# Kernel tuning notes

Hardware: AMD Instinct MI355X
Metric: run time of the kernel (lower is better)

Reference implementation:

```python
import jax, jax.numpy as jnp
import numpy as np


def setup_inputs() -> dict:
    key = jax.random.key(0)
    k1, k2 = jax.random.split(key)
    B, H, W, C = 16, 1024, 1024, 3
    image = jax.random.normal(k1, (B, H, W, C), dtype=jnp.float32)
    flow = jax.random.normal(k2, (B, H, W, 2), dtype=jnp.float32)
    return {"image": image, "flow": flow}


def reference(image, flow):
    # Backward warp: out(p) = bilinear_sample(image, p + flow(p)).
    # NOTE: the original build() swaps width/height (width=shape[1], height=shape[2]);
    # this is only consistent for square images (H == W), which we assume here.
    B, H, W, C = image.shape
    grid_x = jnp.arange(W, dtype=jnp.float32)[None, None, :]  # [1,1,W]
    grid_y = jnp.arange(H, dtype=jnp.float32)[None, :, None]  # [1,H,1]
    x = grid_x + flow[..., 0]  # [B,H,W]
    y = grid_y + flow[..., 1]
    # normalize to [-1,1] then back (faithful to original round-trip)
    x = 0.5 * (2.0 * (x / W - 0.5) + 1.0) * W
    y = 0.5 * (2.0 * (y / H - 0.5) + 1.0) * H
    # corner indices (tf.cast truncates toward zero, as does astype(int32))
    x0 = x.astype(jnp.int32)
    x1 = x0 + 1
    y0 = y.astype(jnp.int32)
    y1 = y0 + 1
    x0 = jnp.clip(x0, 0, W - 1)
    x1 = jnp.clip(x1, 0, W - 1)
    y0 = jnp.clip(y0, 0, H - 1)
    y1 = jnp.clip(y1, 0, H - 1)
    # flat gather indices into [B*H*W, C] image, matching the 4 tf.gather calls
    base = (jnp.arange(B, dtype=jnp.int32) * (H * W))[:, None, None]  # [B,1,1]
    flat_img = image.reshape(B * H * W, C)
    ia = (base + y0 * W + x0).reshape(-1)
    ib = (base + y1 * W + x0).reshape(-1)
    ic = (base + y0 * W + x1).reshape(-1)
    idd = (base + y1 * W + x1).reshape(-1)
    pa = flat_img[ia]  # [B*H*W, C]
    pb = flat_img[ib]
    pc = flat_img[ic]
    pd = flat_img[idd]
    # bilinear blend weights from clipped corner coords (as in original)
    x0f = x0.astype(jnp.float32).reshape(-1)
    x1f = x1.astype(jnp.float32).reshape(-1)
    y0f = y0.astype(jnp.float32).reshape(-1)
    y1f = y1.astype(jnp.float32).reshape(-1)
    xf = x.reshape(-1)
    yf = y.reshape(-1)
    wa = ((x1f - xf) * (y1f - yf))[:, None]
    wb = ((x1f - xf) * (yf - y0f))[:, None]
    wc = ((xf - x0f) * (y1f - yf))[:, None]
    wd = ((xf - x0f) * (yf - y0f))[:, None]
    out = wa * pa + wb * pb + wc * pc + wd * pd
    return out.reshape(B, H, W, C)
```

## Files before the change

### kernel.cpp

```cpp
#include <hip/hip_runtime.h>


struct __attribute__((packed, aligned(4))) R6 { float v[6]; };

__global__ __launch_bounds__(256) void backwarp_kernel(
    const float* __restrict__ image,
    const float* __restrict__ flow,
    float* __restrict__ out) {
  constexpr int H = 1024, W = 1024;
  constexpr int NB = 16 * 1024 * 1024 / 256;
  constexpr int CHUNK = NB / 8;

  int bid = blockIdx.x;
  int sb = (bid & 7) * CHUNK + (bid >> 3);
  int idx = sb * 256 + threadIdx.x;

  int w  = idx & (W - 1);
  int h  = (idx >> 10) & (H - 1);
  int b  = idx >> 20;
  int plane = b << 20;

  float2 f = *reinterpret_cast<const float2*>(flow + (size_t)idx * 2);

  float x = (float)w + f.x;
  float y = (float)h + f.y;
  x = 0.5f * (2.0f * (x * (1.0f / W) - 0.5f) + 1.0f) * W;
  y = 0.5f * (2.0f * (y * (1.0f / H) - 0.5f) + 1.0f) * H;

  int x0 = (int)x;
  int y0 = (int)y;
  int x1 = x0 + 1;
  int y1 = y0 + 1;
  x0 = min(max(x0, 0), W - 1);
  x1 = min(max(x1, 0), W - 1);
  y0 = min(max(y0, 0), H - 1);
  y1 = min(max(y1, 0), H - 1);

  float wa = ((float)x1 - x) * ((float)y1 - y);
  float wb = ((float)x1 - x) * (y - (float)y0);
  float wc = (x - (float)x0) * ((float)y1 - y);
  float wd = (x - (float)x0) * (y - (float)y0);

  int bx = min(x0, W - 2);
  bool hiA = (x0 != bx);
  bool hiC = (x1 != bx);

  const R6 r0 = *reinterpret_cast<const R6*>(image + (size_t)(plane + (y0 << 10) + bx) * 3);
  const R6 r1 = *reinterpret_cast<const R6*>(image + (size_t)(plane + (y1 << 10) + bx) * 3);

  float* o = out + (size_t)idx * 3;
#pragma unroll
  for (int c = 0; c < 3; ++c) {
    float pa  = hiA ? r0.v[3 + c] : r0.v[c];
    float pc_ = hiC ? r0.v[3 + c] : r0.v[c];
    float pb  = hiA ? r1.v[3 + c] : r1.v[c];
    float pd  = hiC ? r1.v[3 + c] : r1.v[c];
    o[c] = wa * pa + wb * pb + wc * pc_ + wd * pd;
  }
}

extern "C" void kernel_launch(void* const* d_in, const int* in_sizes, int n_in,
                              void* d_out, int out_size, void* d_ws, size_t ws_size,
                              hipStream_t stream) {
  const float* image = (const float*)d_in[0];
  const float* flow  = (const float*)d_in[1];
  float* out = (float*)d_out;

  const int total = 16 * 1024 * 1024;
  const int block = 256;
  const int grid = total / block;
  backwarp_kernel<<<grid, block, 0, stream>>>(image, flow, out);
}
```

Before: 156.6 us.

## Process 2x2 pixels per thread in 64x16 tiles with nontemporal vector I/O

Each block now covers a 64x16 pixel tile instead of a 256-pixel row segment, and each thread computes a 2x2 pixel quad. That cuts the grid to 16384 blocks. Flow is read as a 16-byte vector per row pair and outputs are written as float4+float2 nontemporal stores. The 2D tiling is meant to improve cache reuse of the gathered image rows and raise per-thread memory-level parallelism. In exchange it uses more registers per thread and has fewer threads overall.

New measurement: 144.7 us. 7.6% less time.

```diff
diff --git a/kernel.cpp b/kernel.cpp
--- a/kernel.cpp
+++ b/kernel.cpp
@@ -2,60 +2,80 @@
 
 
 struct __attribute__((packed, aligned(4))) R6 { float v[6]; };
+typedef float f4 __attribute__((ext_vector_type(4), aligned(8)));
+typedef float f2 __attribute__((ext_vector_type(2), aligned(8)));
 
 __global__ __launch_bounds__(256) void backwarp_kernel(
     const float* __restrict__ image,
     const float* __restrict__ flow,
     float* __restrict__ out) {
   constexpr int H = 1024, W = 1024;
-  constexpr int NB = 16 * 1024 * 1024 / 256;
+  constexpr int NB = 16384;
   constexpr int CHUNK = NB / 8;
 
   int bid = blockIdx.x;
   int sb = (bid & 7) * CHUNK + (bid >> 3);
-  int idx = sb * 256 + threadIdx.x;
 
-  int w  = idx & (W - 1);
-  int h  = (idx >> 10) & (H - 1);
-  int b  = idx >> 20;
+  int b      = sb >> 10;
+  int r      = sb & 1023;
+  int tile_x = r >> 6;
+  int tile_y = r & 63;
+
+  int qx = threadIdx.x & 31;
+  int qy = threadIdx.x >> 5;
+  int w0 = (tile_x << 6) + (qx << 1);
+  int h0 = (tile_y << 4) + (qy << 1);
   int plane = b << 20;
 
-  float2 f = *reinterpret_cast<const float2*>(flow + (size_t)idx * 2);
+#pragma unroll
+  for (int dy = 0; dy < 2; ++dy) {
+    int h = h0 + dy;
+    int idx0 = plane + (h << 10) + w0;
+    f4 fl = __builtin_nontemporal_load(
+        reinterpret_cast<const f4*>(flow + (size_t)idx0 * 2));
+    float res[6];
+#pragma unroll
+    for (int dx = 0; dx < 2; ++dx) {
+      float x = (float)(w0 + dx) + (dx ? fl.z : fl.x);
+      float y = (float)h + (dx ? fl.w : fl.y);
+      x = 0.5f * (2.0f * (x * (1.0f / W) - 0.5f) + 1.0f) * W;
+      y = 0.5f * (2.0f * (y * (1.0f / H) - 0.5f) + 1.0f) * H;
 
-  float x = (float)w + f.x;
-  float y = (float)h + f.y;
-  x = 0.5f * (2.0f * (x * (1.0f / W) - 0.5f) + 1.0f) * W;
-  y = 0.5f * (2.0f * (y * (1.0f / H) - 0.5f) + 1.0f) * H;
+      int x0 = (int)x;
+      int y0 = (int)y;
+      int x1 = x0 + 1;
+      int y1 = y0 + 1;
+      x0 = min(max(x0, 0), W - 1);
+      x1 = min(max(x1, 0), W - 1);
+      y0 = min(max(y0, 0), H - 1);
+      y1 = min(max(y1, 0), H - 1);
 
-  int x0 = (int)x;
-  int y0 = (int)y;
-  int x1 = x0 + 1;
-  int y1 = y0 + 1;
-  x0 = min(max(x0, 0), W - 1);
-  x1 = min(max(x1, 0), W - 1);
-  y0 = min(max(y0, 0), H - 1);
-  y1 = min(max(y1, 0), H - 1);
+      float wa = ((float)x1 - x) * ((float)y1 - y);
+      float wb = ((float)x1 - x) * (y - (float)y0);
+      float wc = (x - (float)x0) * ((float)y1 - y);
+      float wd = (x - (float)x0) * (y - (float)y0);
 
-  float wa = ((float)x1 - x) * ((float)y1 - y);
-  float wb = ((float)x1 - x) * (y - (float)y0);
-  float wc = (x - (float)x0) * ((float)y1 - y);
-  float wd = (x - (float)x0) * (y - (float)y0);
+      int bx = min(x0, W - 2);
+      bool hiA = (x0 != bx);
+      bool hiC = (x1 != bx);
 
-  int bx = min(x0, W - 2);
-  bool hiA = (x0 != bx);
-  bool hiC = (x1 != bx);
+      const R6 r0 = *reinterpret_cast<const R6*>(image + (size_t)(plane + (y0 << 10) + bx) * 3);
+      const R6 r1 = *reinterpret_cast<const R6*>(image + (size_t)(plane + (y1 << 10) + bx) * 3);
 
-  const R6 r0 = *reinterpret_cast<const R6*>(image + (size_t)(plane + (y0 << 10) + bx) * 3);
-  const R6 r1 = *reinterpret_cast<const R6*>(image + (size_t)(plane + (y1 << 10) + bx) * 3);
-
-  float* o = out + (size_t)idx * 3;
 #pragma unroll
-  for (int c = 0; c < 3; ++c) {
-    float pa  = hiA ? r0.v[3 + c] : r0.v[c];
-    float pc_ = hiC ? r0.v[3 + c] : r0.v[c];
-    float pb  = hiA ? r1.v[3 + c] : r1.v[c];
-    float pd  = hiC ? r1.v[3 + c] : r1.v[c];
-    o[c] = wa * pa + wb * pb + wc * pc_ + wd * pd;
+      for (int c = 0; c < 3; ++c) {
+        float pa  = hiA ? r0.v[3 + c] : r0.v[c];
+        float pc_ = hiC ? r0.v[3 + c] : r0.v[c];
+        float pb  = hiA ? r1.v[3 + c] : r1.v[c];
+        float pd  = hiC ? r1.v[3 + c] : r1.v[c];
+        res[dx * 3 + c] = wa * pa + wb * pb + wc * pc_ + wd * pd;
+      }
+    }
+    float* o = out + (size_t)idx0 * 3;
+    f4 s0 = {res[0], res[1], res[2], res[3]};
+    f2 s1 = {res[4], res[5]};
+    __builtin_nontemporal_store(s0, reinterpret_cast<f4*>(o));
+    __builtin_nontemporal_store(s1, reinterpret_cast<f2*>(o + 4));
   }
 }
 
@@ -66,8 +86,5 @@
   const float* flow  = (const float*)d_in[1];
   float* out = (float*)d_out;
 
-  const int total = 16 * 1024 * 1024;
-  const int block = 256;
-  const int grid = total / block;
-  backwarp_kernel<<<grid, block, 0, stream>>>(image, flow, out);
+  backwarp_kernel<<<16384, 256, 0, stream>>>(image, flow, out);
 }
```
